# Performance work log

Measured on AMD Instinct MI355X. Metric: run time of the kernel, lower is better.

Reference implementation:

```python
import jax, jax.numpy as jnp
import numpy as np

B, S, D, H, DH = 2, 4096, 768, 12, 64

def setup_inputs() -> dict:
    key = jax.random.key(0)
    kx, kq, kk, kv = jax.random.split(key, 4)
    x = jax.random.normal(kx, (B, S, D), dtype=jnp.float32)
    # per-head Q/K/V projection weights, stacked over heads: [H, d_in, d_out]
    Wq = jax.random.normal(kq, (H, D, DH), dtype=jnp.float32) * 0.02
    Wk = jax.random.normal(kk, (H, D, DH), dtype=jnp.float32) * 0.02
    Wv = jax.random.normal(kv, (H, D, DH), dtype=jnp.float32) * 0.02
    return {"x": x, "Wq": Wq, "Wk": Wk, "Wv": Wv}

def reference(x, Wq, Wk, Wv):
    b, s, _ = x.shape
    # per-head linear projections (qkv_bias=False), batched over heads
    q = jnp.einsum('bsd,hde->bhse', x, Wq)  # [B,H,S,DH]
    k = jnp.einsum('bsd,hde->bhse', x, Wk)
    v = jnp.einsum('bsd,hde->bhse', x, Wv)
    scale = 1.0 / jnp.sqrt(jnp.asarray(q.shape[-1], q.dtype))
    scores = jnp.einsum('bhqe,bhke->bhqk', q, k) * scale  # [B,H,S,S]
    causal_mask = jnp.triu(jnp.ones((s, s), dtype=bool), k=1)
    scores = jnp.where(causal_mask, -jnp.inf, scores)
    attn = jax.nn.softmax(scores, axis=-1)  # dropout p=0 -> identity
    ctx = jnp.einsum('bhqk,bhke->bhqe', attn, v)  # [B,H,S,DH]
    # concat heads on last dim (matches torch.cat of per-head outputs)
    return ctx.transpose(0, 2, 1, 3).reshape(b, s, -1)  # [B,S,H*DH]
```

## Files before the change

### kernel.cpp

```cpp
#include <hip/hip_runtime.h>
#include <hip/hip_bf16.h>
#include <stdint.h>

#define B_  2
#define S_  4096
#define D_  768
#define H_  12
#define DH_ 64
#define BS_ (B_*S_)

typedef __bf16 bf16x8 __attribute__((ext_vector_type(8)));
typedef short  svec8  __attribute__((ext_vector_type(8)));
typedef float  fvec4  __attribute__((ext_vector_type(4)));
typedef int    ivec4  __attribute__((ext_vector_type(4)));
typedef unsigned short ushort_t;

__device__ __forceinline__ ushort_t bfc(float f){
    return __builtin_bit_cast(ushort_t, (__bf16)f);
}

__device__ __forceinline__ unsigned cvt_pk_bf16(float lo, float hi){
    unsigned r;
    asm("v_cvt_pk_bf16_f32 %0, %1, %2" : "=v"(r) : "v"(lo), "v"(hi));
    return r;
}

__device__ __forceinline__ fvec4 mfma16(svec8 a, svec8 b, fvec4 c){
    return __builtin_amdgcn_mfma_f32_16x16x32_bf16(
        __builtin_bit_cast(bf16x8, a), __builtin_bit_cast(bf16x8, b), c, 0, 0, 0);
}

__global__ __launch_bounds__(256) void prep(
    const float* __restrict__ X,
    const float* __restrict__ Wq, const float* __restrict__ Wk, const float* __restrict__ Wv,
    ushort_t* __restrict__ Xb, ushort_t* __restrict__ Wsz)
{
    const int bid = blockIdx.x;
    if (bid < 3072) {
        size_t idx = ((size_t)bid * 256 + threadIdx.x) * 8;
        float4 d0 = *(const float4*)(X + idx);
        float4 d1 = *(const float4*)(X + idx + 4);
        bf16x8 pk;
        pk[0] = (__bf16)d0.x; pk[1] = (__bf16)d0.y;
        pk[2] = (__bf16)d0.z; pk[3] = (__bf16)d0.w;
        pk[4] = (__bf16)d1.x; pk[5] = (__bf16)d1.y;
        pk[6] = (__bf16)d1.z; pk[7] = (__bf16)d1.w;
        *(svec8*)(Xb + idx) = __builtin_bit_cast(svec8, pk);
    } else {
        const int v  = bid - 3072;
        const int wt = v % 3;
        const int hk = v / 3;
        const int h  = hk / 12, kt = hk % 12;
        const float* W  = (wt == 0) ? Wq : (wt == 1) ? Wk : Wv;
        const float* Wh = W + (size_t)h * (D_ * DH_) + (size_t)kt * 64 * DH_;
        ushort_t* dst = Wsz + (size_t)(hk * 3 + wt) * 4096;
        #pragma unroll
        for (int i = 0; i < 16; i++) {
            int idx = threadIdx.x * 16 + i;
            int k = idx >> 6, n = idx & 63;
            float val = Wh[k * DH_ + n];
            int addr = n * 64 + ((((k >> 3) ^ ((n >> 2) & 7))) << 3) + (k & 7);
            dst[addr] = bfc(val);
        }
    }
}

__global__ __launch_bounds__(256, 3) void qkv_proj(
    const ushort_t* __restrict__ Xb, const ushort_t* __restrict__ Wsz,
    ushort_t* __restrict__ Qb, ushort_t* __restrict__ Kb, ushort_t* __restrict__ Vg)
{
    const int m0 = blockIdx.x * 128;
    const int h  = blockIdx.y;

    __shared__ ushort_t smem[128 * 72 + 3 * 4096];
    ushort_t* Xs  = smem;
    ushort_t* Wts = smem + 128 * 72;
    ushort_t* XsT = smem;

    const int tid  = threadIdx.x;
    const int w    = tid >> 6;
    const int lane = tid & 63;
    const int quad = lane >> 4;
    const int l15  = lane & 15;

    fvec4 acc[3][2][4];
    #pragma unroll
    for (int wt = 0; wt < 3; wt++)
        #pragma unroll
        for (int i = 0; i < 2; i++)
            #pragma unroll
            for (int j = 0; j < 4; j++) acc[wt][i][j] = (fvec4){0.f, 0.f, 0.f, 0.f};

    for (int kt = 0; kt < 12; kt++) {
        const int k0 = kt * 64;
        #pragma unroll
        for (int i = 0; i < 4; i++) {
            int v = tid + 256 * i;
            int r = v >> 3, c = (v & 7) * 8;
            *(svec8*)(Xs + r * 72 + c) =
                *(const svec8*)(Xb + (size_t)(m0 + r) * D_ + k0 + c);
        }
        const ushort_t* wsrc = Wsz + (size_t)(h * 12 + kt) * 3 * 4096;
        #pragma unroll
        for (int j = 0; j < 6; j++) {
            int lin = (tid + 256 * j) * 8;
            *(svec8*)(Wts + lin) = *(const svec8*)(wsrc + lin);
        }
        __syncthreads();

        #pragma unroll
        for (int ks = 0; ks < 2; ks++) {
            svec8 a0 = *(const svec8*)(Xs + (32 * w + l15) * 72 + ks * 32 + quad * 8);
            svec8 a1 = *(const svec8*)(Xs + (32 * w + 16 + l15) * 72 + ks * 32 + quad * 8);
            #pragma unroll
            for (int wt = 0; wt < 3; wt++)
                #pragma unroll
                for (int ns = 0; ns < 4; ns++) {
                    int n = ns * 16 + l15;
                    int swz = (ks * 4 + quad) ^ ((n >> 2) & 7);
                    svec8 b = *(const svec8*)(Wts + wt * 4096 + n * 64 + swz * 8);
                    acc[wt][0][ns] = mfma16(a0, b, acc[wt][0][ns]);
                    acc[wt][1][ns] = mfma16(a1, b, acc[wt][1][ns]);
                }
        }
        __syncthreads();
    }

    const float qs = 0.18033688011112042f;
    #pragma unroll
    for (int ms = 0; ms < 2; ms++)
        #pragma unroll
        for (int ns = 0; ns < 4; ns++)
            #pragma unroll
            for (int r = 0; r < 4; r++) {
                int row = m0 + 32 * w + ms * 16 + quad * 4 + r;
                int col = h * DH_ + ns * 16 + l15;
                Qb[(size_t)row * D_ + col] = bfc(acc[0][ms][ns][r] * qs);
                Kb[(size_t)row * D_ + col] = bfc(acc[1][ms][ns][r]);
            }
    #pragma unroll
    for (int ms = 0; ms < 2; ms++)
        #pragma unroll
        for (int ns = 0; ns < 4; ns++)
            #pragma unroll
            for (int r = 0; r < 4; r++) {
                int sl = 32 * w + ms * 16 + quad * 4 + r;
                int e  = ns * 16 + l15;
                XsT[e * 136 + sl] = bfc(acc[2][ms][ns][r]);
            }
    __syncthreads();
    #pragma unroll
    for (int i = 0; i < 4; i++) {
        int v = tid + 256 * i;
        int e = v >> 4, s0 = (v & 15) * 8;
        svec8 d = *(const svec8*)(XsT + e * 136 + s0);
        *(svec8*)(Vg + (size_t)(h * DH_ + e) * BS_ + m0 + s0) = d;
    }
}

__global__ __launch_bounds__(256, 5) void attn(
    const ushort_t* __restrict__ Qb, const ushort_t* __restrict__ Kb,
    const ushort_t* __restrict__ Vg, float* __restrict__ Out)
{
    const int fid = blockIdx.x;
    const int qt  = (S_ / 64 - 1) - fid / (H_ * B_);
    const int r24 = fid % (H_ * B_);
    const int h   = r24 % H_;
    const int b   = r24 / H_;
    const int q0 = qt * 64;

    const int tid  = threadIdx.x;
    const int w    = tid >> 6;
    const int lane = tid & 63;
    const int quad = lane >> 4;
    const int l15  = lane & 15;

    __shared__ ushort_t Ks[64 * 72];
    __shared__ ushort_t Vt[64 * 72];

    const size_t hb = (size_t)b * S_ * D_ + (size_t)h * DH_;
    const ushort_t* Vh = Vg + (size_t)h * DH_ * BS_ + (size_t)b * S_;

    const int sr = tid >> 3;
    const int sc = (tid & 7) * 8;
    const int pr0 = (((sr      >> 2) & 1) << 5) | (((sr      >> 5) & 1) << 4) |
                    (((sr      >> 4) & 1) << 3) | (((sr      >> 3) & 1) << 2) | (sr & 3);
    const int sr1 = sr + 32;
    const int pr1 = (((sr1 >> 2) & 1) << 5) | (((sr1 >> 5) & 1) << 4) |
                    (((sr1 >> 4) & 1) << 3) | (((sr1 >> 3) & 1) << 2) | (sr1 & 3);

    svec8 aq[2];
    {
        const ushort_t* qrow = Qb + hb + (size_t)(q0 + 16 * w + l15) * D_;
        aq[0] = *(const svec8*)(qrow + quad * 8);
        aq[1] = *(const svec8*)(qrow + 32 + quad * 8);
    }

    float m_i = -INFINITY;
    float ls  = 0.f;
    fvec4 acc[4];
    #pragma unroll
    for (int n = 0; n < 4; n++) acc[n] = (fvec4){0.f, 0.f, 0.f, 0.f};

    const ushort_t* kp = Kb + hb + (size_t)sr * D_ + sc;
    const ushort_t* vp = Vh + (size_t)sr * BS_ + sc;

    svec8 kd[2], vd[2];
    kd[0] = *(const svec8*)(kp);
    kd[1] = *(const svec8*)(kp + (size_t)32 * D_);
    vd[0] = *(const svec8*)(vp);
    vd[1] = *(const svec8*)(vp + (size_t)32 * BS_);
    kp += (size_t)64 * D_;
    vp += 64;
    *(svec8*)(Ks + pr0 * 72 + sc) = kd[0];
    *(svec8*)(Ks + pr1 * 72 + sc) = kd[1];
    *(svec8*)(Vt + sr  * 72 + sc) = vd[0];
    *(svec8*)(Vt + sr1 * 72 + sc) = vd[1];

    for (int kt = 0; kt <= qt; ++kt) {
        __syncthreads();

        if (kt < qt) {
            kd[0] = *(const svec8*)(kp);
            kd[1] = *(const svec8*)(kp + (size_t)32 * D_);
            vd[0] = *(const svec8*)(vp);
            vd[1] = *(const svec8*)(vp + (size_t)32 * BS_);
            kp += (size_t)64 * D_;
            vp += 64;
        }

        fvec4 st[4];
        #pragma unroll
        for (int n = 0; n < 4; n++) st[n] = (fvec4){0.f, 0.f, 0.f, 0.f};
        #pragma unroll
        for (int ks = 0; ks < 2; ks++)
            #pragma unroll
            for (int n = 0; n < 4; n++) {
                svec8 ka = *(const svec8*)(Ks + (n * 16 + l15) * 72 + ks * 32 + quad * 8);
                st[n] = mfma16(ka, aq[ks], st[n]);
            }

        if (kt == qt) {
            #pragma unroll
            for (int n = 0; n < 4; n++)
                #pragma unroll
                for (int r = 0; r < 4; r++) {
                    int key = (n & 1) * 32 + quad * 8 + (n >> 1) * 4 + r;
                    int row = 16 * w + l15;
                    if (key > row) st[n][r] = -INFINITY;
                }
        }

        float mxa = fmaxf(fmaxf(st[0][0], st[0][1]), st[0][2]);
        mxa = fmaxf(fmaxf(mxa, st[0][3]), st[1][0]);
        mxa = fmaxf(fmaxf(mxa, st[1][1]), st[1][2]);
        mxa = fmaxf(mxa, st[1][3]);
        float mxb = fmaxf(fmaxf(st[2][0], st[2][1]), st[2][2]);
        mxb = fmaxf(fmaxf(mxb, st[2][3]), st[3][0]);
        mxb = fmaxf(fmaxf(mxb, st[3][1]), st[3][2]);
        mxb = fmaxf(mxb, st[3][3]);
        float mx = fmaxf(mxa, mxb);
        mx = fmaxf(mx, __shfl_xor(mx, 16));
        mx = fmaxf(mx, __shfl_xor(mx, 32));

        if (__any(mx > m_i)) {
            float mn = fmaxf(m_i, mx);
            float alpha = exp2f(m_i - mn);
            m_i = mn;
            ls *= alpha;
            float ar[4];
            #pragma unroll
            for (int r = 0; r < 4; r++)
                ar[r] = __shfl(alpha, quad * 16 + quad * 4 + r);
            #pragma unroll
            for (int n = 0; n < 4; n++)
                #pragma unroll
                for (int r = 0; r < 4; r++) acc[n][r] *= ar[r];
        }

        ivec4 ai0, ai1;
        float psum[4];
        #pragma unroll
        for (int n = 0; n < 4; n++) {
            float p0 = exp2f(st[n][0] - m_i);
            float p1 = exp2f(st[n][1] - m_i);
            float p2 = exp2f(st[n][2] - m_i);
            float p3 = exp2f(st[n][3] - m_i);
            psum[n] = (p0 + p1) + (p2 + p3);
            unsigned d0 = cvt_pk_bf16(p0, p1);
            unsigned d1 = cvt_pk_bf16(p2, p3);
            if (n == 0)      { ai0[0] = (int)d0; ai0[1] = (int)d1; }
            else if (n == 1) { ai1[0] = (int)d0; ai1[1] = (int)d1; }
            else if (n == 2) { ai0[2] = (int)d0; ai0[3] = (int)d1; }
            else             { ai1[2] = (int)d0; ai1[3] = (int)d1; }
        }
        ls += (psum[0] + psum[2]) + (psum[1] + psum[3]);
        svec8 ap0 = __builtin_bit_cast(svec8, ai0);
        svec8 ap1 = __builtin_bit_cast(svec8, ai1);

        #pragma unroll
        for (int ks = 0; ks < 2; ks++) {
            svec8 ap = ks ? ap1 : ap0;
            #pragma unroll
            for (int n = 0; n < 4; n++) {
                svec8 bv = *(const svec8*)(Vt + (n * 16 + l15) * 72 + ks * 32 + quad * 8);
                acc[n] = mfma16(ap, bv, acc[n]);
            }
        }

        __syncthreads();

        if (kt < qt) {
            *(svec8*)(Ks + pr0 * 72 + sc) = kd[0];
            *(svec8*)(Ks + pr1 * 72 + sc) = kd[1];
            *(svec8*)(Vt + sr  * 72 + sc) = vd[0];
            *(svec8*)(Vt + sr1 * 72 + sc) = vd[1];
        }
    }

    float lsum = ls;
    lsum += __shfl_xor(lsum, 16);
    lsum += __shfl_xor(lsum, 32);
    float li[4];
    #pragma unroll
    for (int r = 0; r < 4; r++)
        li[r] = __shfl(lsum, quad * 16 + quad * 4 + r);
    #pragma unroll
    for (int n = 0; n < 4; n++)
        #pragma unroll
        for (int r = 0; r < 4; r++) {
            int row = q0 + 16 * w + quad * 4 + r;
            int col = h * DH_ + n * 16 + l15;
            Out[((size_t)b * S_ + row) * D_ + col] = acc[n][r] / li[r];
        }
}

extern "C" void kernel_launch(void* const* d_in, const int* in_sizes, int n_in,
                              void* d_out, int out_size, void* d_ws, size_t ws_size,
                              hipStream_t stream)
{
    const float* X  = (const float*)d_in[0];
    const float* Wq = (const float*)d_in[1];
    const float* Wk = (const float*)d_in[2];
    const float* Wv = (const float*)d_in[3];

    ushort_t* Qb = (ushort_t*)d_ws;
    ushort_t* Kb = Qb + (size_t)BS_ * D_;
    ushort_t* Vg = Kb + (size_t)BS_ * D_;

    ushort_t* Xb  = (ushort_t*)d_out;
    ushort_t* Wsz = Xb + (size_t)BS_ * D_;
    float* Out = (float*)d_out;

    prep<<<dim3(3072 + 432), dim3(256), 0, stream>>>(X, Wq, Wk, Wv, Xb, Wsz);
    qkv_proj<<<dim3(64, H_), dim3(256), 0, stream>>>(Xb, Wsz, Qb, Kb, Vg);
    attn<<<dim3((S_ / 64) * H_ * B_), dim3(256), 0, stream>>>(Qb, Kb, Vg, Out);
}
```

Baseline: 246.7 us.

## Use fragment-ordered LDS layout and register-prefetch X tiles in QKV projection

Changes the pre-swizzled weight layout and the X shared-memory tile to an MFMA-fragment-contiguous order, so each lane reads its operand with a simple linear offset. This drops the padded 72-stride layout and the per-access XOR address arithmetic. It also prefetches the next X k-tile into registers while the current tile is being computed, overlapping global loads with MFMA work. The cost is more register use and shared-memory write patterns that may cause bank conflicts.

```diff
diff --git a/kernel.cpp b/kernel.cpp
--- a/kernel.cpp
+++ b/kernel.cpp
@@ -59,7 +59,8 @@
             int idx = threadIdx.x * 16 + i;
             int k = idx >> 6, n = idx & 63;
             float val = Wh[k * DH_ + n];
-            int addr = n * 64 + ((((k >> 3) ^ ((n >> 2) & 7))) << 3) + (k & 7);
+            int addr = (((k >> 5) * 4 + (n >> 4)) * 64 + (n & 15) * 4 + ((k >> 3) & 3)) * 8
+                     + (k & 7);
             dst[addr] = bfc(val);
         }
     }
@@ -72,9 +73,9 @@
     const int m0 = blockIdx.x * 128;
     const int h  = blockIdx.y;
 
-    __shared__ ushort_t smem[128 * 72 + 3 * 4096];
+    __shared__ ushort_t smem[128 * 64 + 3 * 4096];
     ushort_t* Xs  = smem;
-    ushort_t* Wts = smem + 128 * 72;
+    ushort_t* Wts = smem + 128 * 64;
     ushort_t* XsT = smem;
 
     const int tid  = threadIdx.x;
@@ -82,6 +83,7 @@
     const int lane = tid & 63;
     const int quad = lane >> 4;
     const int l15  = lane & 15;
+    const int lp8  = (l15 * 4 + quad) * 8;
 
     fvec4 acc[3][2][4];
     #pragma unroll
@@ -91,34 +93,49 @@
             #pragma unroll
             for (int j = 0; j < 4; j++) acc[wt][i][j] = (fvec4){0.f, 0.f, 0.f, 0.f};
 
+    const ushort_t* xsrc = Xb + (size_t)m0 * D_;
+    const ushort_t* wsrc = Wsz + (size_t)(h * 12) * 3 * 4096;
+
+    int xr[4], xdu[4];
+    #pragma unroll
+    for (int i = 0; i < 4; i++) {
+        int v = tid + 256 * i;
+        int r = v >> 3, t = v & 7;
+        xr[i]  = r * D_ + t * 8;
+        xdu[i] = (((r >> 4) * 2 + (t >> 2)) * 64 + (r & 15) * 4 + (t & 3)) * 8;
+    }
+
+    svec8 xd[4];
+    #pragma unroll
+    for (int i = 0; i < 4; i++) xd[i] = *(const svec8*)(xsrc + xr[i]);
+
     for (int kt = 0; kt < 12; kt++) {
-        const int k0 = kt * 64;
-        #pragma unroll
-        for (int i = 0; i < 4; i++) {
-            int v = tid + 256 * i;
-            int r = v >> 3, c = (v & 7) * 8;
-            *(svec8*)(Xs + r * 72 + c) =
-                *(const svec8*)(Xb + (size_t)(m0 + r) * D_ + k0 + c);
-        }
-        const ushort_t* wsrc = Wsz + (size_t)(h * 12 + kt) * 3 * 4096;
-        #pragma unroll
-        for (int j = 0; j < 6; j++) {
-            int lin = (tid + 256 * j) * 8;
-            *(svec8*)(Wts + lin) = *(const svec8*)(wsrc + lin);
-        }
+        const ushort_t* wp = wsrc + (size_t)kt * 3 * 4096;
+        svec8 wd[6];
+        #pragma unroll
+        for (int j = 0; j < 6; j++)
+            wd[j] = *(const svec8*)(wp + (tid + 256 * j) * 8);
+        #pragma unroll
+        for (int i = 0; i < 4; i++) *(svec8*)(Xs + xdu[i]) = xd[i];
+        #pragma unroll
+        for (int j = 0; j < 6; j++) *(svec8*)(Wts + (tid + 256 * j) * 8) = wd[j];
         __syncthreads();
 
+        if (kt < 11) {
+            #pragma unroll
+            for (int i = 0; i < 4; i++)
+                xd[i] = *(const svec8*)(xsrc + xr[i] + (kt + 1) * 64);
+        }
+
         #pragma unroll
         for (int ks = 0; ks < 2; ks++) {
-            svec8 a0 = *(const svec8*)(Xs + (32 * w + l15) * 72 + ks * 32 + quad * 8);
-            svec8 a1 = *(const svec8*)(Xs + (32 * w + 16 + l15) * 72 + ks * 32 + quad * 8);
+            svec8 a0 = *(const svec8*)(Xs + (4 * w + ks) * 512 + lp8);
+            svec8 a1 = *(const svec8*)(Xs + (4 * w + 2 + ks) * 512 + lp8);
             #pragma unroll
             for (int wt = 0; wt < 3; wt++)
                 #pragma unroll
                 for (int ns = 0; ns < 4; ns++) {
-                    int n = ns * 16 + l15;
-                    int swz = (ks * 4 + quad) ^ ((n >> 2) & 7);
-                    svec8 b = *(const svec8*)(Wts + wt * 4096 + n * 64 + swz * 8);
+                    svec8 b = *(const svec8*)(Wts + (wt * 8 + ks * 4 + ns) * 512 + lp8);
                     acc[wt][0][ns] = mfma16(a0, b, acc[wt][0][ns]);
                     acc[wt][1][ns] = mfma16(a1, b, acc[wt][1][ns]);
                 }
```

After: 219.4 us. 1.12x faster.
